# Performance work log

Measured on AMD Instinct MI355X. Metric: run time of the kernel, lower is better.

The kernel has to match this reference:

```python
import jax, jax.numpy as jnp
import numpy as np

E = 8            # num_experts
H = 1024         # hidden_size
I = 1024         # moe_intermediate_dim
T = 8192         # total tokens (sum of per-expert counts; no padding, grouped_mm path)
# Imbalanced routing, sums exactly to T
COUNTS = np.array([512, 1536, 1024, 768, 1280, 896, 1152, 1024], dtype=np.int32)


def setup_inputs() -> dict:
    key = jax.random.key(0)
    k_x, k_gu, k_d = jax.random.split(key, 3)
    x = jax.random.normal(k_x, (T, H), dtype=jnp.float32)
    # Weights stored pre-transposed: (E, H, 2I) and (E, I, H)
    gate_up_proj = jax.random.normal(k_gu, (E, H, 2 * I), dtype=jnp.float32) * (1.0 / np.sqrt(H))
    down_proj = jax.random.normal(k_d, (E, I, H), dtype=jnp.float32) * (1.0 / np.sqrt(I))
    num_tokens_per_expert = jnp.asarray(COUNTS)  # int32, sums to T
    return {
        "x": x,
        "gate_up_proj": gate_up_proj,
        "down_proj": down_proj,
        "num_tokens_per_expert": num_tokens_per_expert,
    }


def reference(x, gate_up_proj, down_proj, num_tokens_per_expert):
    # Grouped GEMM 1: [T,H] x [E,H,2I] with ragged group sizes -> [T,2I]
    gate_up = jax.lax.ragged_dot(x, gate_up_proj, group_sizes=num_tokens_per_expert)
    gate, up = jnp.split(gate_up, 2, axis=-1)
    h = jax.nn.silu(gate) * up  # SwiGLU: silu(gate) * up, [T,I]
    # Grouped GEMM 2: [T,I] x [E,I,H] -> [T,H]
    out = jax.lax.ragged_dot(h, down_proj, group_sizes=num_tokens_per_expert)
    return out.astype(x.dtype)
```

## Files before the change

kernel.cpp:

```cpp
#include <hip/hip_runtime.h>
#include <hip/hip_bf16.h>
#include <stdint.h>

#define E_ 8
#define H_ 1024
#define I_ 1024
#define T_ 8192
#define BM 128
#define BK 32
#define NKT 32

typedef __attribute__((ext_vector_type(4))) float f32x4;
typedef __attribute__((ext_vector_type(8))) short bf16x8;
typedef __attribute__((ext_vector_type(8))) unsigned short u16x8;

__device__ __forceinline__ unsigned short f2bf(float f) {
  union { float f; unsigned int u; } v; v.f = f;
  unsigned int lsb = (v.u >> 16) & 1u;
  v.u += 0x7fffu + lsb;
  return (unsigned short)(v.u >> 16);
}

__device__ __forceinline__ void gload_lds16(const void* g, void* l) {
  __builtin_amdgcn_global_load_lds(
      (const __attribute__((address_space(1))) unsigned int*)g,
      (__attribute__((address_space(3))) unsigned int*)l,
      16, 0, 0);
}

__device__ __forceinline__ void find_tile(const int* counts, int ty,
                                          int& row_start, int& rows, int& expert) {
  int tacc = 0, off = 0;
  expert = 0; row_start = 0; rows = BM;
  #pragma unroll
  for (int e = 0; e < E_; ++e) {
    int c = counts[e];
    int te = (c + BM - 1) >> 7;
    if (ty >= tacc && ty < tacc + te) {
      expert = e;
      int lt = ty - tacc;
      row_start = off + lt * BM;
      rows = min(BM, c - lt * BM);
    }
    tacc += te; off += c;
  }
}

__device__ __forceinline__ void transpose_role(const float* __restrict__ inp,
                                               unsigned short* __restrict__ outp,
                                               int R, int C, int bx, int by,
                                               float* tile ) {
  int c0 = bx * 64, r0 = by * 128;
  int lc = threadIdx.x & 15;
  int lrw = threadIdx.x >> 4;
  #pragma unroll
  for (int p = 0; p < 8; ++p) {
    int r = p * 16 + lrw;
    float4 v = *reinterpret_cast<const float4*>(
        inp + (size_t)(r0 + r) * C + c0 + lc * 4);
    float* t = &tile[r * 65 + lc * 4];
    t[0] = v.x; t[1] = v.y; t[2] = v.z; t[3] = v.w;
  }
  __syncthreads();
  int lq = threadIdx.x & 15;
  int co = threadIdx.x >> 4;
  #pragma unroll
  for (int p = 0; p < 4; ++p) {
    int cc = p * 16 + co;
    u16x8 o;
    #pragma unroll
    for (int i = 0; i < 8; ++i)
      o[i] = f2bf(tile[(8 * lq + i) * 65 + cc]);
    *reinterpret_cast<u16x8*>(&outp[(size_t)(c0 + cc) * R + r0 + 8 * lq]) = o;
  }
}

__global__ __launch_bounds__(256) void preproc_all(
    const float* __restrict__ x, unsigned short* __restrict__ xb,
    const float* __restrict__ w1, unsigned short* __restrict__ w1t,
    const float* __restrict__ w2, unsigned short* __restrict__ w2t) {
  __shared__ float tile[128 * 65];
  int id = blockIdx.x;
  if (id < 2048) {
    #pragma unroll
    for (int it = 0; it < 4; ++it) {
      int i = id * 4096 + it * 1024 + threadIdx.x * 4;
      float4 v = *reinterpret_cast<const float4*>(x + i);
      ushort4 o;
      o.x = f2bf(v.x); o.y = f2bf(v.y); o.z = f2bf(v.z); o.w = f2bf(v.w);
      *reinterpret_cast<ushort4*>(xb + i) = o;
    }
    return;
  }
  if (id < 4096) {
    int tb = id - 2048;
    int bx = tb & 31, by = (tb >> 5) & 7, bz = tb >> 8;
    transpose_role(w1 + (size_t)bz * H_ * 2 * I_,
                   w1t + (size_t)bz * H_ * 2 * I_, H_, 2 * I_, bx, by, tile);
    return;
  }
  int tb = id - 4096;
  int bx = tb & 15, by = (tb >> 4) & 7, bz = tb >> 7;
  transpose_role(w2 + (size_t)bz * I_ * H_,
                 w2t + (size_t)bz * I_ * H_, I_, H_, bx, by, tile);
}

#define GLDS (BM * BK + 256 * BK)
__global__ __launch_bounds__(256, 2) void gemm1_swiglu(
    const unsigned short* __restrict__ X,
    const unsigned short* __restrict__ W1T,
    const int* __restrict__ counts,
    unsigned short* __restrict__ Hout) {
  __shared__ unsigned short pool[3 * GLDS];
  int id = blockIdx.x;
  int swz = (id & 7) * 64 + (id >> 3);
  int bn = swz & 7;
  int tyid = swz >> 3;
  int row_start, rows, expert;
  find_tile(counts, tyid, row_start, rows, expert);
  int tid = threadIdx.x, wid = tid >> 6, lane = tid & 63;
  const unsigned short* Wp = W1T + (size_t)expert * (2 * I_) * H_;

  f32x4 acc[8][4];
  #pragma unroll
  for (int m = 0; m < 8; ++m)
    #pragma unroll
    for (int n = 0; n < 4; ++n) acc[m][n] = {0.f, 0.f, 0.f, 0.f};

  int l4 = lane >> 2;
  int csw = ((lane & 3) ^ ((l4 >> 1) & 3)) * 8;
  int lr = lane & 15;
  int ck = ((lane >> 4) ^ ((lr >> 1) & 3)) * 8;

#define STAGE1(buf, kt) do {                                                   \
    int k0 = (kt) * BK + csw;                                                  \
    unsigned short* Ab = pool + (buf) * GLDS;                                  \
    unsigned short* Bb = Ab + BM * BK;                                         \
    _Pragma("unroll")                                                          \
    for (int i = 0; i < 2; ++i) {                                              \
      int r = wid * 32 + i * 16;                                               \
      int gr = row_start + min(r + l4, rows - 1);                              \
      gload_lds16(X + (size_t)gr * H_ + k0, Ab + r * BK);                      \
    }                                                                          \
    _Pragma("unroll")                                                          \
    for (int i = 0; i < 4; ++i) {                                              \
      int r = wid * 64 + i * 16;                                               \
      int rb = r + l4;                                                         \
      int sub = rb & 63, ow = rb >> 6;                                         \
      int col = (sub < 32) ? (bn * 128 + ow * 32 + sub)                        \
                           : (I_ + bn * 128 + ow * 32 + sub - 32);             \
      gload_lds16(Wp + (size_t)col * H_ + k0, Bb + r * BK);                    \
    }                                                                          \
  } while (0)

  STAGE1(0, 0);
  STAGE1(1, 1);
  for (int kt = 0; kt < NKT; ++kt) {
    STAGE1((kt + 2) % 3, min(kt + 2, NKT - 1));
    asm volatile("s_waitcnt vmcnt(12)" ::: "memory");
    __builtin_amdgcn_sched_barrier(0);
    __builtin_amdgcn_s_barrier();
    const unsigned short* Ab = pool + (kt % 3) * GLDS;
    const unsigned short* Bb = Ab + BM * BK;
    bf16x8 a[8], b[4];
    #pragma unroll
    for (int m = 0; m < 8; ++m)
      a[m] = *reinterpret_cast<const bf16x8*>(&Ab[(m * 16 + lr) * BK + ck]);
    #pragma unroll
    for (int n = 0; n < 4; ++n)
      b[n] = *reinterpret_cast<const bf16x8*>(&Bb[(wid * 64 + n * 16 + lr) * BK + ck]);
    __builtin_amdgcn_s_setprio(1);
    #pragma unroll
    for (int m = 0; m < 8; ++m)
      #pragma unroll
      for (int n = 0; n < 4; ++n)
        acc[m][n] = __builtin_amdgcn_mfma_f32_16x16x32_bf16(a[m], b[n], acc[m][n], 0, 0, 0);
    __builtin_amdgcn_s_setprio(0);
    __builtin_amdgcn_s_barrier();
  }
#undef STAGE1

  int lq = lane >> 4;
  #pragma unroll
  for (int m = 0; m < 8; ++m)
    #pragma unroll
    for (int n = 0; n < 2; ++n) {
      f32x4 g = acc[m][n], u = acc[m][n + 2];
      #pragma unroll
      for (int r = 0; r < 4; ++r) {
        int rl = m * 16 + lq * 4 + r;
        if (rl < rows) {
          float gv = g[r];
          float hv = (gv / (1.f + __expf(-gv))) * u[r];
          Hout[(size_t)(row_start + rl) * I_ + bn * 128 + wid * 32 + n * 16 + lr] = f2bf(hv);
        }
      }
    }
}

#define GBUF 24576
#define GNKT 16

__device__ __forceinline__ bf16x8 ldfrag(const unsigned short* b, int row, int ck) {
  return *reinterpret_cast<const bf16x8*>(&b[row * 64 + ck]);
}

__global__ __launch_bounds__(512, 1) void gemm2(
    const unsigned short* __restrict__ Hin,
    const unsigned short* __restrict__ W2T,
    const int* __restrict__ counts,
    float* __restrict__ Out) {
  __shared__ unsigned short pool[3 * GBUF];
  int id = blockIdx.x;
  int swz = (id & 7) * 32 + (id >> 3);
  int bn = swz & 3;
  int tyid = swz >> 2;
  int row_start, rows, expert;
  find_tile(counts, tyid, row_start, rows, expert);
  int tid = threadIdx.x, w = tid >> 6, lane = tid & 63;
  int wr = w >> 2, wc = w & 3;
  const unsigned short* Wp = W2T + (size_t)expert * H_ * I_;

  f32x4 acc[4][4];
  #pragma unroll
  for (int m = 0; m < 4; ++m)
    #pragma unroll
    for (int n = 0; n < 4; ++n) acc[m][n] = {0.f, 0.f, 0.f, 0.f};

  int lr = lane & 15, hi = lane >> 4;
  int ck0 = (hi ^ (lr & 7)) * 8;
  int ck1 = ((4 + hi) ^ (lr & 7)) * 8;
  int sr = lane >> 3;
  int cgo = ((lane & 7) ^ sr) * 8;

#define S2A(buf, kt, i) do {                                                   \
    int r = (w * 2 + (i)) * 8 + sr;                                            \
    int gr = row_start + min(r, rows - 1);                                     \
    gload_lds16(Hin + (size_t)gr * I_ + (kt) * 64 + cgo,                       \
                pool + (buf) * GBUF + (w * 2 + (i)) * 512);                    \
  } while (0)
#define S2B(buf, kt, i) do {                                                   \
    int rb = (w * 4 + (i)) * 8 + sr;                                           \
    int col = bn * 256 + rb;                                                   \
    gload_lds16(Wp + (size_t)col * I_ + (kt) * 64 + cgo,                       \
                pool + (buf) * GBUF + 8192 + (w * 4 + (i)) * 512);             \
  } while (0)

  S2A(0, 0, 0); S2A(0, 0, 1); S2B(0, 0, 0); S2B(0, 0, 1); S2B(0, 0, 2); S2B(0, 0, 3);
  S2A(1, 1, 0); S2A(1, 1, 1); S2B(1, 1, 0); S2B(1, 1, 1); S2B(1, 1, 2); S2B(1, 1, 3);
  asm volatile("s_waitcnt vmcnt(6)" ::: "memory");
  __builtin_amdgcn_sched_barrier(0);
  __builtin_amdgcn_s_barrier();

  for (int t = 0; t < GNKT; ++t) {
    const unsigned short* Ab = pool + (t % 3) * GBUF;
    const unsigned short* Bb = Ab + 8192;
    int dst = (t + 2) % 3;
    int nk = t + 2;
    bool pre = (nk < GNKT);
    bf16x8 bf[4], af[2];
    #pragma unroll
    for (int n = 0; n < 4; ++n) bf[n] = ldfrag(Bb, wc * 64 + n * 16 + lr, ck0);
    af[0] = ldfrag(Ab, wr * 64 + lr, ck0);
    af[1] = ldfrag(Ab, wr * 64 + 16 + lr, ck0);
    if (pre) S2A(dst, nk, 0);
    __builtin_amdgcn_s_barrier();
    __builtin_amdgcn_s_setprio(1);
    #pragma unroll
    for (int m = 0; m < 2; ++m)
      #pragma unroll
      for (int n = 0; n < 4; ++n)
        acc[m][n] = __builtin_amdgcn_mfma_f32_16x16x32_bf16(af[m], bf[n], acc[m][n], 0, 0, 0);
    __builtin_amdgcn_s_setprio(0);
    __builtin_amdgcn_s_barrier();
    af[0] = ldfrag(Ab, wr * 64 + 32 + lr, ck0);
    af[1] = ldfrag(Ab, wr * 64 + 48 + lr, ck0);
    if (pre) S2A(dst, nk, 1);
    __builtin_amdgcn_s_barrier();
    __builtin_amdgcn_s_setprio(1);
    #pragma unroll
    for (int m = 0; m < 2; ++m)
      #pragma unroll
      for (int n = 0; n < 4; ++n)
        acc[m + 2][n] = __builtin_amdgcn_mfma_f32_16x16x32_bf16(af[m], bf[n], acc[m + 2][n], 0, 0, 0);
    __builtin_amdgcn_s_setprio(0);
    __builtin_amdgcn_s_barrier();
    #pragma unroll
    for (int n = 0; n < 4; ++n) bf[n] = ldfrag(Bb, wc * 64 + n * 16 + lr, ck1);
    af[0] = ldfrag(Ab, wr * 64 + lr, ck1);
    af[1] = ldfrag(Ab, wr * 64 + 16 + lr, ck1);
    if (pre) { S2B(dst, nk, 0); S2B(dst, nk, 1); }
    __builtin_amdgcn_s_barrier();
    __builtin_amdgcn_s_setprio(1);
    #pragma unroll
    for (int m = 0; m < 2; ++m)
      #pragma unroll
      for (int n = 0; n < 4; ++n)
        acc[m][n] = __builtin_amdgcn_mfma_f32_16x16x32_bf16(af[m], bf[n], acc[m][n], 0, 0, 0);
    __builtin_amdgcn_s_setprio(0);
    __builtin_amdgcn_s_barrier();
    af[0] = ldfrag(Ab, wr * 64 + 32 + lr, ck1);
    af[1] = ldfrag(Ab, wr * 64 + 48 + lr, ck1);
    if (pre) {
      S2B(dst, nk, 2); S2B(dst, nk, 3);
      asm volatile("s_waitcnt vmcnt(6)" ::: "memory");
    } else {
      asm volatile("s_waitcnt vmcnt(0)" ::: "memory");
    }
    __builtin_amdgcn_sched_barrier(0);
    __builtin_amdgcn_s_barrier();
    __builtin_amdgcn_s_setprio(1);
    #pragma unroll
    for (int m = 0; m < 2; ++m)
      #pragma unroll
      for (int n = 0; n < 4; ++n)
        acc[m + 2][n] = __builtin_amdgcn_mfma_f32_16x16x32_bf16(af[m], bf[n], acc[m + 2][n], 0, 0, 0);
    __builtin_amdgcn_s_setprio(0);
    __builtin_amdgcn_s_barrier();
  }
#undef S2A
#undef S2B

  int lq = lane >> 4;
  #pragma unroll
  for (int m = 0; m < 4; ++m)
    #pragma unroll
    for (int n = 0; n < 4; ++n)
      #pragma unroll
      for (int r = 0; r < 4; ++r) {
        int rl = wr * 64 + m * 16 + lq * 4 + r;
        if (rl < rows)
          Out[(size_t)(row_start + rl) * H_ + bn * 256 + wc * 64 + n * 16 + lr] =
              acc[m][n][r];
      }
}

extern "C" void kernel_launch(void* const* d_in, const int* in_sizes, int n_in,
                              void* d_out, int out_size, void* d_ws, size_t ws_size,
                              hipStream_t stream) {
  const float* x  = (const float*)d_in[0];
  const float* w1 = (const float*)d_in[1];
  const float* w2 = (const float*)d_in[2];
  const int* counts = (const int*)d_in[3];
  float* out = (float*)d_out;

  char* ws = (char*)d_ws;
  unsigned short* xb  = (unsigned short*)ws;
  unsigned short* w1t = (unsigned short*)(ws + (size_t)T_ * H_ * 2);
  unsigned short* w2t = (unsigned short*)(ws + (size_t)T_ * H_ * 2
                                             + (size_t)E_ * 2 * I_ * H_ * 2);
  unsigned short* hbuf = (unsigned short*)(ws + (size_t)T_ * H_ * 2
                                              + (size_t)E_ * 2 * I_ * H_ * 2
                                              + (size_t)E_ * H_ * I_ * 2);

  preproc_all<<<5120, 256, 0, stream>>>(x, xb, w1, w1t, w2, w2t);
  gemm1_swiglu<<<512, 256, 0, stream>>>(xb, w1t, counts, hbuf);
  gemm2<<<256, 512, 0, stream>>>(hbuf, w2t, counts, out);
}
```

Measured before the change: 100.9 us.

## Fuse fp32-to-bf16 conversion of activations into GEMM1 A-tile loading

Removes the separate x conversion from the preprocessing kernel. GEMM1 now loads fp32 rows of x into registers, converts them to bf16 and writes them into swizzled LDS, replacing the direct global-to-LDS bf16 load. This saves writing and re-reading a bf16 copy of x. In exchange, GEMM1 reads twice the bytes per A tile, spends extra VALU and register work, and has a more involved wait-count pipeline, and each x row is re-read by all 8 column blocks.

```diff
diff --git a/kernel.cpp b/kernel.cpp
--- a/kernel.cpp
+++ b/kernel.cpp
@@ -75,31 +75,18 @@
   }
 }
 
-__global__ __launch_bounds__(256) void preproc_all(
-    const float* __restrict__ x, unsigned short* __restrict__ xb,
+__global__ __launch_bounds__(256) void preproc_w(
     const float* __restrict__ w1, unsigned short* __restrict__ w1t,
     const float* __restrict__ w2, unsigned short* __restrict__ w2t) {
   __shared__ float tile[128 * 65];
   int id = blockIdx.x;
   if (id < 2048) {
-    #pragma unroll
-    for (int it = 0; it < 4; ++it) {
-      int i = id * 4096 + it * 1024 + threadIdx.x * 4;
-      float4 v = *reinterpret_cast<const float4*>(x + i);
-      ushort4 o;
-      o.x = f2bf(v.x); o.y = f2bf(v.y); o.z = f2bf(v.z); o.w = f2bf(v.w);
-      *reinterpret_cast<ushort4*>(xb + i) = o;
-    }
-    return;
-  }
-  if (id < 4096) {
-    int tb = id - 2048;
-    int bx = tb & 31, by = (tb >> 5) & 7, bz = tb >> 8;
+    int bx = id & 31, by = (id >> 5) & 7, bz = id >> 8;
     transpose_role(w1 + (size_t)bz * H_ * 2 * I_,
                    w1t + (size_t)bz * H_ * 2 * I_, H_, 2 * I_, bx, by, tile);
     return;
   }
-  int tb = id - 4096;
+  int tb = id - 2048;
   int bx = tb & 15, by = (tb >> 4) & 7, bz = tb >> 7;
   transpose_role(w2 + (size_t)bz * I_ * H_,
                  w2t + (size_t)bz * I_ * H_, I_, H_, bx, by, tile);
@@ -107,7 +94,7 @@
 
 #define GLDS (BM * BK + 256 * BK)
 __global__ __launch_bounds__(256, 2) void gemm1_swiglu(
-    const unsigned short* __restrict__ X,
+    const float* __restrict__ X32,
     const unsigned short* __restrict__ W1T,
     const int* __restrict__ counts,
     unsigned short* __restrict__ Hout) {
@@ -132,16 +119,41 @@
   int lr = lane & 15;
   int ck = ((lane >> 4) ^ ((lr >> 1) & 3)) * 8;
 
-#define STAGE1(buf, kt) do {                                                   \
+  int ar = tid >> 1;
+  int ah = tid & 1;
+  int agr = row_start + min(ar, rows - 1);
+  const float* aptr = X32 + (size_t)agr * H_ + ah * 16;
+  int asw = (ar >> 1) & 3;
+  int ap0 = ((2 * ah) ^ asw) * 8;
+  int ap1 = ((2 * ah + 1) ^ asw) * 8;
+  float4 areg[4];
+
+#define A_LOAD(kt) do {                                                        \
+    const float* p_ = aptr + (kt) * BK;                                        \
+    areg[0] = *reinterpret_cast<const float4*>(p_);                            \
+    areg[1] = *reinterpret_cast<const float4*>(p_ + 4);                        \
+    areg[2] = *reinterpret_cast<const float4*>(p_ + 8);                        \
+    areg[3] = *reinterpret_cast<const float4*>(p_ + 12);                       \
+  } while (0)
+
+#define A_WRITE(buf) do {                                                      \
+    unsigned short* Ab_ = pool + (buf) * GLDS;                                 \
+    u16x8 o0, o1;                                                              \
+    o0[0] = f2bf(areg[0].x); o0[1] = f2bf(areg[0].y);                          \
+    o0[2] = f2bf(areg[0].z); o0[3] = f2bf(areg[0].w);                          \
+    o0[4] = f2bf(areg[1].x); o0[5] = f2bf(areg[1].y);                          \
+    o0[6] = f2bf(areg[1].z); o0[7] = f2bf(areg[1].w);                          \
+    o1[0] = f2bf(areg[2].x); o1[1] = f2bf(areg[2].y);                          \
+    o1[2] = f2bf(areg[2].z); o1[3] = f2bf(areg[2].w);                          \
+    o1[4] = f2bf(areg[3].x); o1[5] = f2bf(areg[3].y);                          \
+    o1[6] = f2bf(areg[3].z); o1[7] = f2bf(areg[3].w);                          \
+    *reinterpret_cast<u16x8*>(&Ab_[ar * BK + ap0]) = o0;                       \
+    *reinterpret_cast<u16x8*>(&Ab_[ar * BK + ap1]) = o1;                       \
+  } while (0)
+
+#define B_STAGE(buf, kt) do {                                                  \
     int k0 = (kt) * BK + csw;                                                  \
-    unsigned short* Ab = pool + (buf) * GLDS;                                  \
-    unsigned short* Bb = Ab + BM * BK;                                         \
-    _Pragma("unroll")                                                          \
-    for (int i = 0; i < 2; ++i) {                                              \
-      int r = wid * 32 + i * 16;                                               \
-      int gr = row_start + min(r + l4, rows - 1);                              \
-      gload_lds16(X + (size_t)gr * H_ + k0, Ab + r * BK);                      \
-    }                                                                          \
+    unsigned short* Bb_ = pool + (buf) * GLDS + BM * BK;                       \
     _Pragma("unroll")                                                          \
     for (int i = 0; i < 4; ++i) {                                              \
       int r = wid * 64 + i * 16;                                               \
@@ -149,15 +161,23 @@
       int sub = rb & 63, ow = rb >> 6;                                         \
       int col = (sub < 32) ? (bn * 128 + ow * 32 + sub)                        \
                            : (I_ + bn * 128 + ow * 32 + sub - 32);             \
-      gload_lds16(Wp + (size_t)col * H_ + k0, Bb + r * BK);                    \
+      gload_lds16(Wp + (size_t)col * H_ + k0, Bb_ + r * BK);                   \
     }                                                                          \
   } while (0)
 
-  STAGE1(0, 0);
-  STAGE1(1, 1);
+  A_LOAD(0);
+  A_WRITE(0);
+  A_LOAD(1);
+  B_STAGE(0, 0);
+  B_STAGE(1, 1);
+
   for (int kt = 0; kt < NKT; ++kt) {
-    STAGE1((kt + 2) % 3, min(kt + 2, NKT - 1));
-    asm volatile("s_waitcnt vmcnt(12)" ::: "memory");
+    asm volatile("s_waitcnt vmcnt(4)" ::: "memory");
+    __builtin_amdgcn_sched_barrier(0);
+    A_WRITE((kt + 1) % 3);
+    A_LOAD(min(kt + 2, NKT - 1));
+    B_STAGE((kt + 2) % 3, min(kt + 2, NKT - 1));
+    asm volatile("s_waitcnt vmcnt(8) lgkmcnt(0)" ::: "memory");
     __builtin_amdgcn_sched_barrier(0);
     __builtin_amdgcn_s_barrier();
     const unsigned short* Ab = pool + (kt % 3) * GLDS;
@@ -178,7 +198,9 @@
     __builtin_amdgcn_s_setprio(0);
     __builtin_amdgcn_s_barrier();
   }
-#undef STAGE1
+#undef A_LOAD
+#undef A_WRITE
+#undef B_STAGE
 
   int lq = lane >> 4;
   #pragma unroll
@@ -345,15 +367,12 @@
   float* out = (float*)d_out;
 
   char* ws = (char*)d_ws;
-  unsigned short* xb  = (unsigned short*)ws;
-  unsigned short* w1t = (unsigned short*)(ws + (size_t)T_ * H_ * 2);
-  unsigned short* w2t = (unsigned short*)(ws + (size_t)T_ * H_ * 2
-                                             + (size_t)E_ * 2 * I_ * H_ * 2);
-  unsigned short* hbuf = (unsigned short*)(ws + (size_t)T_ * H_ * 2
-                                              + (size_t)E_ * 2 * I_ * H_ * 2
+  unsigned short* w1t = (unsigned short*)ws;
+  unsigned short* w2t = (unsigned short*)(ws + (size_t)E_ * 2 * I_ * H_ * 2);
+  unsigned short* hbuf = (unsigned short*)(ws + (size_t)E_ * 2 * I_ * H_ * 2
                                               + (size_t)E_ * H_ * I_ * 2);
 
-  preproc_all<<<5120, 256, 0, stream>>>(x, xb, w1, w1t, w2, w2t);
-  gemm1_swiglu<<<512, 256, 0, stream>>>(xb, w1t, counts, hbuf);
+  preproc_w<<<3072, 256, 0, stream>>>(w1, w1t, w2, w2t);
+  gemm1_swiglu<<<512, 256, 0, stream>>>(x, w1t, counts, hbuf);
   gemm2<<<256, 512, 0, stream>>>(hbuf, w2t, counts, out);
 }
```

Result: no change. 98.99 us (-1.9%).
